# Kernel tuning notes

Hardware: AMD Instinct MI355X
Metric: run time of the kernel (lower is better)

Reference implementation:

```python
import jax, jax.numpy as jnp
import numpy as np

B, N, D = 4, 4096, 1024
DFF = 4 * D
K = 2048  # max(1, int(N * 0.5))


def setup_inputs() -> dict:
    key = jax.random.key(0)
    ks = jax.random.split(key, 4)
    x = jax.random.normal(ks[0], (B, N, D), dtype=jnp.float32)
    gate_w = jax.random.normal(ks[1], (1, D), dtype=jnp.float32) * 0.02
    w1 = jax.random.normal(ks[2], (D, DFF), dtype=jnp.float32) * (1.0 / np.sqrt(D))
    b1 = jnp.zeros((DFF,), dtype=jnp.float32)
    w2 = jax.random.normal(ks[3], (DFF, D), dtype=jnp.float32) * (1.0 / np.sqrt(DFF))
    b2 = jnp.zeros((D,), dtype=jnp.float32)
    return {"x": x, "gate_w": gate_w, "w1": w1, "b1": b1, "w2": w2, "b2": b2, "k": K}


def reference(x, gate_w, w1, b1, w2, b2, k):
    # scores: [B, N] = gate(x).squeeze(-1)
    scores = jnp.einsum("bnd,d->bn", x, gate_w[0])
    _, topk = jax.lax.top_k(scores, k)          # [B, k] token indices
    # gather selected tokens: [B, k, D]
    x_sel = jnp.take_along_axis(x, topk[:, :, None], axis=1)
    # ffn (d -> 4d -> d, GELU) + residual on selected tokens only
    h = jax.nn.gelu(x_sel @ w1 + b1) @ w2 + b2
    x_proc = x_sel + h
    # scatter processed tokens back into a copy of x
    b_idx = jnp.arange(x.shape[0])[:, None]      # [B, 1]
    out = x.at[b_idx, topk].set(x_proc)
    return out
```

## Files before the change

### kernel.cpp

```cpp
#include <hip/hip_runtime.h>
#include <math.h>

#define B_   4
#define N_   4096
#define D_   1024
#define DFF_ 4096
#define K_   2048

typedef __attribute__((ext_vector_type(8))) short short8;
typedef __attribute__((ext_vector_type(4))) float float4v;

__device__ __forceinline__ unsigned short f2bf(float f) {
    unsigned int u = __float_as_uint(f);
    u = (u + 0x7fffu + ((u >> 16) & 1u)) >> 16;
    return (unsigned short)u;
}

__device__ __forceinline__ void gld16(const void* g, void* l) {
    __builtin_amdgcn_global_load_lds((const __attribute__((address_space(1))) void*)g,
                                     (__attribute__((address_space(3))) void*)l, 16, 0, 0);
}

__global__ __launch_bounds__(256) void scores_kernel(const float* __restrict__ x,
                                                     const float* __restrict__ gate_w,
                                                     float* __restrict__ scores,
                                                     int* __restrict__ slot) {
    int wave = (blockIdx.x * blockDim.x + threadIdx.x) >> 6;
    int lane = threadIdx.x & 63;
    if (wave >= B_ * N_) return;
    if (lane == 1) slot[wave] = -1;
    const float4* xr = (const float4*)(x + (size_t)wave * D_);
    const float4* g  = (const float4*)gate_w;
    float acc = 0.f;
    #pragma unroll
    for (int j = 0; j < D_ / 4 / 64; ++j) {
        float4 a = xr[lane + j * 64];
        float4 b = g[lane + j * 64];
        acc += a.x * b.x + a.y * b.y + a.z * b.z + a.w * b.w;
    }
    #pragma unroll
    for (int off = 32; off > 0; off >>= 1) acc += __shfl_down(acc, off, 64);
    if (lane == 0) scores[wave] = acc;
}

__global__ __launch_bounds__(1024) void select_topk_kernel(const float* __restrict__ scores,
                                                           int* __restrict__ topk,
                                                           int* __restrict__ slot) {
    __shared__ unsigned key[N_];
    __shared__ unsigned hist[256];
    __shared__ int sh_bin, sh_rem, sh_ngt;
    __shared__ int wsum[16], woff[16];
    int b = blockIdx.x, tid = threadIdx.x;
    int lane = tid & 63, wid = tid >> 6;

    for (int i = tid; i < N_; i += 1024) {
        unsigned u = __float_as_uint(scores[b * N_ + i]);
        key[i] = (u & 0x80000000u) ? ~u : (u | 0x80000000u);
    }
    if (tid == 0) sh_ngt = 0;
    __syncthreads();

    unsigned prefix = 0, pmask = 0;
    int rem = K_;
    for (int shift = 24; shift >= 0; shift -= 8) {
        if (tid < 256) hist[tid] = 0;
        __syncthreads();
        for (int i = tid; i < N_; i += 1024) {
            unsigned k = key[i];
            if ((k & pmask) == prefix) atomicAdd(&hist[(k >> shift) & 255u], 1u);
        }
        __syncthreads();
        if (tid < 64) {
            unsigned v0 = hist[4 * lane], v1 = hist[4 * lane + 1];
            unsigned v2 = hist[4 * lane + 2], v3 = hist[4 * lane + 3];
            unsigned s3 = v3, s2 = v2 + s3, s1 = v1 + s2, s0 = v0 + s1;
            unsigned t = s0;
            #pragma unroll
            for (int off = 1; off < 64; off <<= 1) {
                unsigned u = __shfl_down(t, off, 64);
                if (lane + off < 64) t += u;
            }
            unsigned above = t - s0;
            unsigned S0 = s0 + above, S1 = s1 + above, S2 = s2 + above, S3 = s3 + above;
            unsigned R = (unsigned)rem;
            if (S0 >= R && S1 < R) { sh_bin = 4 * lane;     sh_rem = rem - (int)S1; }
            if (S1 >= R && S2 < R) { sh_bin = 4 * lane + 1; sh_rem = rem - (int)S2; }
            if (S2 >= R && S3 < R) { sh_bin = 4 * lane + 2; sh_rem = rem - (int)S3; }
            if (S3 >= R && above < R) { sh_bin = 4 * lane + 3; sh_rem = rem - (int)above; }
        }
        __syncthreads();
        prefix |= ((unsigned)sh_bin) << shift;
        pmask  |= 0xffu << shift;
        rem = sh_rem;
    }
    unsigned T = prefix;
    int c_gt = K_ - rem;

    for (int i = tid; i < N_; i += 1024) {
        bool p = key[i] > T;
        unsigned long long m = __ballot(p);
        int cnt = __popcll(m);
        int basepos = 0;
        if (lane == 0 && cnt) basepos = atomicAdd(&sh_ngt, cnt);
        basepos = __shfl(basepos, 0, 64);
        if (p) {
            int pos = basepos + __popcll(m & ((1ULL << lane) - 1ULL));
            topk[b * K_ + pos] = i;
            slot[b * N_ + i] = b * K_ + pos;
        }
    }
    int base = tid * 4, c = 0;
    #pragma unroll
    for (int j = 0; j < 4; ++j) c += (key[base + j] == T);
    int sc = c;
    #pragma unroll
    for (int off = 1; off < 64; off <<= 1) {
        int u = __shfl_up(sc, off, 64);
        if (lane >= off) sc += u;
    }
    if (lane == 63) wsum[wid] = sc;
    __syncthreads();
    if (tid == 0) {
        int run = 0;
        #pragma unroll
        for (int j = 0; j < 16; ++j) { woff[j] = run; run += wsum[j]; }
    }
    __syncthreads();
    int r = woff[wid] + sc - c;
    #pragma unroll
    for (int j = 0; j < 4; ++j) {
        if (key[base + j] == T) {
            if (r < rem) {
                topk[b * K_ + c_gt + r] = base + j;
                slot[b * N_ + base + j] = b * K_ + c_gt + r;
            }
            ++r;
        }
    }
}

__global__ __launch_bounds__(256) void gather_copy_kernel(const float* __restrict__ x,
                                                          const int* __restrict__ slot,
                                                          unsigned short* __restrict__ xsel,
                                                          float* __restrict__ out) {
    int row = blockIdx.x;
    int t = threadIdx.x;
    int s = slot[row];
    float4 v = ((const float4*)(x + (size_t)row * D_))[t];
    if (s >= 0) {
        ushort4 o;
        o.x = f2bf(v.x); o.y = f2bf(v.y); o.z = f2bf(v.z); o.w = f2bf(v.w);
        ((ushort4*)(xsel + (size_t)s * D_))[t] = o;
    } else {
        ((float4*)(out + (size_t)row * D_))[t] = v;
    }
}

__global__ __launch_bounds__(256) void transpose_both_kernel(const float* __restrict__ w1,
                                                             const float* __restrict__ w2,
                                                             unsigned short* __restrict__ w1t,
                                                             unsigned short* __restrict__ w2t) {
    __shared__ float tile[32][33];
    int bid = blockIdx.x;
    const float* src; unsigned short* dst; int R, C, bx, by;
    if (bid < 4096) { src = w1; dst = w1t; R = D_;   C = DFF_; bx = bid & 127;          by = bid >> 7; }
    else            { src = w2; dst = w2t; R = DFF_; C = D_;   bx = (bid - 4096) & 31;  by = (bid - 4096) >> 5; }
    int tx = threadIdx.x & 31, ty = threadIdx.x >> 5;
    int c = bx * 32 + tx, r0 = by * 32;
    #pragma unroll
    for (int j = ty; j < 32; j += 8) tile[j][tx] = src[(size_t)(r0 + j) * C + c];
    __syncthreads();
    int dc = by * 32 + tx, dr0 = bx * 32;
    #pragma unroll
    for (int j = ty; j < 32; j += 8) dst[(size_t)(dr0 + j) * R + dc] = f2bf(tile[tx][j]);
}

__global__ __launch_bounds__(512, 2) void ffn1_pipe_kernel(const unsigned short* __restrict__ A,
                                                           const unsigned short* __restrict__ Bt,
                                                           const float* __restrict__ b1,
                                                           unsigned short* __restrict__ h1) {
    constexpr int K  = D_;
    constexpr int NT = K / 32;
    __shared__ __align__(16) unsigned short smem[65536];

    const int t    = threadIdx.x;
    const int lane = t & 63;
    const int wid  = t >> 6;
    const int quad = lane >> 4;
    const int lr   = lane & 15;
    const int wr   = wid >> 2;
    const int wc   = wid & 3;
    const int row0 = blockIdx.x * 256;
    const int col0 = blockIdx.y * 256;

    const int ch0 = t, ch1 = t + 512;
    const int r0 = ch0 >> 2, c0 = (ch0 & 3) ^ (r0 & 3);
    const int r1 = ch1 >> 2, c1 = (ch1 & 3) ^ (r1 & 3);
    const char* aS0 = (const char*)A  + ((size_t)(row0 + r0) * K + (size_t)c0 * 8) * 2;
    const char* aS1 = (const char*)A  + ((size_t)(row0 + r1) * K + (size_t)c1 * 8) * 2;
    const char* bS0 = (const char*)Bt + ((size_t)(col0 + r0) * K + (size_t)c0 * 8) * 2;
    const char* bS1 = (const char*)Bt + ((size_t)(col0 + r1) * K + (size_t)c1 * 8) * 2;
    const int oA0 = ch0 * 8, oA1 = ch1 * 8;
    const int oB0 = 8192 + ch0 * 8, oB1 = 8192 + ch1 * 8;

    const int sw   = ((quad ^ (lr & 3)) * 8);
    const int aoff = (wr * 128 + lr) * 32 + sw;
    const int boff = 8192 + (wc * 64 + lr) * 32 + sw;

    #pragma unroll
    for (int pt = 0; pt < 3; ++pt) {
        unsigned short* buf = smem + pt * 16384;
        gld16(aS0, buf + oA0); gld16(aS1, buf + oA1);
        gld16(bS0, buf + oB0); gld16(bS1, buf + oB1);
        aS0 += 64; aS1 += 64; bS0 += 64; bS1 += 64;
    }
    asm volatile("s_waitcnt vmcnt(8)" ::: "memory");
    __builtin_amdgcn_s_barrier();

    float4v acc[8][4] = {};
    short8 af[8], bq[4];

    #pragma unroll 4
    for (int kt = 0; kt < NT; ++kt) {
        unsigned short* cur = smem + (kt & 3) * 16384;
        unsigned short* nxt = smem + ((kt + 3) & 3) * 16384;
        const bool pf = (kt + 3 < NT);

        #pragma unroll
        for (int mi = 0; mi < 4; ++mi) af[mi] = *(const short8*)(cur + aoff + mi * 512);
        #pragma unroll
        for (int ni = 0; ni < 4; ++ni) bq[ni] = *(const short8*)(cur + boff + ni * 512);
        if (pf) { gld16(aS0, nxt + oA0); gld16(aS1, nxt + oA1); }
        __builtin_amdgcn_s_barrier();
        __builtin_amdgcn_s_setprio(1);
        #pragma unroll
        for (int mi = 0; mi < 4; ++mi)
            #pragma unroll
            for (int ni = 0; ni < 4; ++ni)
                acc[mi][ni] = __builtin_amdgcn_mfma_f32_16x16x32_bf16(af[mi], bq[ni], acc[mi][ni], 0, 0, 0);
        __builtin_amdgcn_s_setprio(0);
        __builtin_amdgcn_s_barrier();

        #pragma unroll
        for (int mi = 4; mi < 8; ++mi) af[mi] = *(const short8*)(cur + aoff + mi * 512);
        if (pf) { gld16(bS0, nxt + oB0); gld16(bS1, nxt + oB1); }
        aS0 += 64; aS1 += 64; bS0 += 64; bS1 += 64;
        if (kt < NT - 3)       asm volatile("s_waitcnt vmcnt(8)" ::: "memory");
        else if (kt == NT - 3) asm volatile("s_waitcnt vmcnt(4)" ::: "memory");
        else                   asm volatile("s_waitcnt vmcnt(0)" ::: "memory");
        __builtin_amdgcn_s_barrier();
        __builtin_amdgcn_s_setprio(1);
        #pragma unroll
        for (int mi = 4; mi < 8; ++mi)
            #pragma unroll
            for (int ni = 0; ni < 4; ++ni)
                acc[mi][ni] = __builtin_amdgcn_mfma_f32_16x16x32_bf16(af[mi], bq[ni], acc[mi][ni], 0, 0, 0);
        __builtin_amdgcn_s_setprio(0);
        __builtin_amdgcn_s_barrier();
    }

    float bias[4];
    #pragma unroll
    for (int ni = 0; ni < 4; ++ni) bias[ni] = b1[col0 + wc * 64 + ni * 16 + lr];
    unsigned short* ws_ = smem + wid * 5120;
    const int ro = row0 + wr * 128;
    const int co = col0 + wc * 64;
    #pragma unroll
    for (int p = 0; p < 2; ++p) {
        #pragma unroll
        for (int mi = 0; mi < 8; ++mi)
            #pragma unroll
            for (int nj = 0; nj < 2; ++nj) {
                const int ni = p * 2 + nj;
                #pragma unroll
                for (int r = 0; r < 4; ++r) {
                    float u = acc[mi][ni][r] + bias[ni];
                    float tt = 1.5957691216057308f * u * (1.0f + 0.044715f * u * u);
                    float g = u / (1.0f + __expf(-tt));
                    ws_[(mi * 16 + quad * 4 + r) * 40 + nj * 16 + lr] = f2bf(g);
                }
            }
        asm volatile("s_waitcnt lgkmcnt(0)" ::: "memory");
        #pragma unroll
        for (int j = 0; j < 8; ++j) {
            const int chk = lane + j * 64;
            const int rr = chk >> 2, cc = chk & 3;
            short8 v = *(const short8*)(ws_ + rr * 40 + cc * 8);
            *(short8*)(h1 + (size_t)(ro + rr) * DFF_ + co + p * 32 + cc * 8) = v;
        }
        asm volatile("s_waitcnt lgkmcnt(0)" ::: "memory");
    }
}

__global__ __launch_bounds__(256) void ffn2_mfma_kernel(const unsigned short* __restrict__ A,
                                                        const unsigned short* __restrict__ Bt,
                                                        const float* __restrict__ b2,
                                                        const float* __restrict__ x,
                                                        const int* __restrict__ topk,
                                                        float* __restrict__ out) {
    constexpr int K = DFF_;
    __shared__ __align__(16) unsigned short As[128 * 32];
    __shared__ __align__(16) unsigned short Bs[128 * 32];
    int t = threadIdx.x;
    int w = t >> 6, lane = t & 63;
    int quad = lane >> 4, lr = lane & 15;
    int wm = w >> 1, wn = w & 1;
    int row0 = blockIdx.x * 128, col0 = blockIdx.y * 128;

    const char* ga0 = (const char*)(A + (size_t)(row0 + (t >> 2)) * K) + (t & 3) * 16;
    const char* ga1 = ga0 + (size_t)64 * K * 2;
    const char* gb0 = (const char*)(Bt + (size_t)(col0 + (t >> 2)) * K) + (t & 3) * 16;
    const char* gb1 = gb0 + (size_t)64 * K * 2;
    unsigned short* la0 = As + t * 8;   unsigned short* la1 = As + 2048 + t * 8;
    unsigned short* lb0 = Bs + t * 8;   unsigned short* lb1 = Bs + 2048 + t * 8;

    float4v acc[4][4] = {};
    for (int k0 = 0; k0 < K; k0 += 32) {
        gld16(ga0, la0); gld16(ga1, la1);
        gld16(gb0, lb0); gld16(gb1, lb1);
        ga0 += 64; ga1 += 64; gb0 += 64; gb1 += 64;
        __syncthreads();
        short8 af[4], bfv[4];
        #pragma unroll
        for (int mi = 0; mi < 4; ++mi)
            af[mi] = *(const short8*)(As + (size_t)(wm * 64 + mi * 16 + lr) * 32 + quad * 8);
        #pragma unroll
        for (int ni = 0; ni < 4; ++ni)
            bfv[ni] = *(const short8*)(Bs + (size_t)(wn * 64 + ni * 16 + lr) * 32 + quad * 8);
        #pragma unroll
        for (int mi = 0; mi < 4; ++mi)
            #pragma unroll
            for (int ni = 0; ni < 4; ++ni)
                acc[mi][ni] = __builtin_amdgcn_mfma_f32_16x16x32_bf16(af[mi], bfv[ni], acc[mi][ni], 0, 0, 0);
        __syncthreads();
    }

    #pragma unroll
    for (int mi = 0; mi < 4; ++mi) {
        #pragma unroll
        for (int r = 0; r < 4; ++r) {
            int row = row0 + wm * 64 + mi * 16 + quad * 4 + r;
            int gb = row >> 11;
            int tok = topk[row];
            size_t base = ((size_t)(gb * N_ + tok)) * D_;
            #pragma unroll
            for (int ni = 0; ni < 4; ++ni) {
                int col = col0 + wn * 64 + ni * 16 + lr;
                out[base + col] = x[base + col] + acc[mi][ni][r] + b2[col];
            }
        }
    }
}

extern "C" void kernel_launch(void* const* d_in, const int* in_sizes, int n_in,
                              void* d_out, int out_size, void* d_ws, size_t ws_size,
                              hipStream_t stream) {
    const float* x      = (const float*)d_in[0];
    const float* gate_w = (const float*)d_in[1];
    const float* w1     = (const float*)d_in[2];
    const float* b1     = (const float*)d_in[3];
    const float* w2     = (const float*)d_in[4];
    const float* b2     = (const float*)d_in[5];
    float* out = (float*)d_out;

    char* ws = (char*)d_ws;
    float*          scores = (float*)ws;
    int*            topk   = (int*)(ws + (64 << 10));
    int*            slot   = (int*)(ws + (96 << 10));
    unsigned short* xsel   = (unsigned short*)(ws + (160 << 10));
    unsigned short* w1t    = (unsigned short*)(ws + (160 << 10) + (16 << 20));
    unsigned short* w2t    = (unsigned short*)(ws + (160 << 10) + (24 << 20));
    unsigned short* h1     = (unsigned short*)(ws + (160 << 10) + (32 << 20));

    scores_kernel<<<(B_ * N_) / 4, 256, 0, stream>>>(x, gate_w, scores, slot);
    select_topk_kernel<<<B_, 1024, 0, stream>>>(scores, topk, slot);

    transpose_both_kernel<<<8192, 256, 0, stream>>>(w1, w2, w1t, w2t);

    gather_copy_kernel<<<B_ * N_, 256, 0, stream>>>(x, slot, xsel, out);

    ffn1_pipe_kernel<<<dim3(32, 16), 512, 0, stream>>>(xsel, w1t, b1, h1);
    ffn2_mfma_kernel<<<dim3(64, 8), 256, 0, stream>>>(h1, w2t, b2, x, topk, out);
}
```

Baseline: 348.3 us.

## Pipeline FFN2 GEMM with 4-stage LDS ring and new LDS swizzle

```diff
diff --git a/kernel.cpp b/kernel.cpp
--- a/kernel.cpp
+++ b/kernel.cpp
@@ -175,6 +175,7 @@
     for (int j = ty; j < 32; j += 8) dst[(size_t)(dr0 + j) * R + dc] = f2bf(tile[tx][j]);
 }
 
+
 __global__ __launch_bounds__(512, 2) void ffn1_pipe_kernel(const unsigned short* __restrict__ A,
                                                            const unsigned short* __restrict__ Bt,
                                                            const float* __restrict__ b1,
@@ -194,18 +195,21 @@
     const int col0 = blockIdx.y * 256;
 
     const int ch0 = t, ch1 = t + 512;
-    const int r0 = ch0 >> 2, c0 = (ch0 & 3) ^ (r0 & 3);
-    const int r1 = ch1 >> 2, c1 = (ch1 & 3) ^ (r1 & 3);
-    const char* aS0 = (const char*)A  + ((size_t)(row0 + r0) * K + (size_t)c0 * 8) * 2;
-    const char* aS1 = (const char*)A  + ((size_t)(row0 + r1) * K + (size_t)c1 * 8) * 2;
-    const char* bS0 = (const char*)Bt + ((size_t)(col0 + r0) * K + (size_t)c0 * 8) * 2;
-    const char* bS1 = (const char*)Bt + ((size_t)(col0 + r1) * K + (size_t)c1 * 8) * 2;
+    const int rp0 = ch0 >> 3, w0 = (ch0 & 7) ^ (rp0 & 7);
+    const int rp1 = ch1 >> 3, w1 = (ch1 & 7) ^ (rp1 & 7);
+    const int gr0 = rp0 * 2 + (w0 >> 2), gc0 = w0 & 3;
+    const int gr1 = rp1 * 2 + (w1 >> 2), gc1 = w1 & 3;
+    const char* aS0 = (const char*)A  + ((size_t)(row0 + gr0) * K + (size_t)gc0 * 8) * 2;
+    const char* aS1 = (const char*)A  + ((size_t)(row0 + gr1) * K + (size_t)gc1 * 8) * 2;
+    const char* bS0 = (const char*)Bt + ((size_t)(col0 + gr0) * K + (size_t)gc0 * 8) * 2;
+    const char* bS1 = (const char*)Bt + ((size_t)(col0 + gr1) * K + (size_t)gc1 * 8) * 2;
     const int oA0 = ch0 * 8, oA1 = ch1 * 8;
     const int oB0 = 8192 + ch0 * 8, oB1 = 8192 + ch1 * 8;
 
-    const int sw   = ((quad ^ (lr & 3)) * 8);
-    const int aoff = (wr * 128 + lr) * 32 + sw;
-    const int boff = 8192 + (wc * 64 + lr) * 32 + sw;
+    const int rbA = wr * 128 + lr, rA2 = rbA >> 1;
+    const int aoff = (rA2 * 8 + ((((rbA & 1) << 2) | quad) ^ (rA2 & 7))) * 8;
+    const int rbB = wc * 64 + lr, rB2 = rbB >> 1;
+    const int boff = 8192 + (rB2 * 8 + ((((rbB & 1) << 2) | quad) ^ (rB2 & 7))) * 8;
 
     #pragma unroll
     for (int pt = 0; pt < 3; ++pt) {
@@ -292,60 +296,104 @@
     }
 }
 
-__global__ __launch_bounds__(256) void ffn2_mfma_kernel(const unsigned short* __restrict__ A,
-                                                        const unsigned short* __restrict__ Bt,
-                                                        const float* __restrict__ b2,
-                                                        const float* __restrict__ x,
-                                                        const int* __restrict__ topk,
-                                                        float* __restrict__ out) {
-    constexpr int K = DFF_;
-    __shared__ __align__(16) unsigned short As[128 * 32];
-    __shared__ __align__(16) unsigned short Bs[128 * 32];
-    int t = threadIdx.x;
-    int w = t >> 6, lane = t & 63;
-    int quad = lane >> 4, lr = lane & 15;
-    int wm = w >> 1, wn = w & 1;
-    int row0 = blockIdx.x * 128, col0 = blockIdx.y * 128;
-
-    const char* ga0 = (const char*)(A + (size_t)(row0 + (t >> 2)) * K) + (t & 3) * 16;
-    const char* ga1 = ga0 + (size_t)64 * K * 2;
-    const char* gb0 = (const char*)(Bt + (size_t)(col0 + (t >> 2)) * K) + (t & 3) * 16;
-    const char* gb1 = gb0 + (size_t)64 * K * 2;
-    unsigned short* la0 = As + t * 8;   unsigned short* la1 = As + 2048 + t * 8;
-    unsigned short* lb0 = Bs + t * 8;   unsigned short* lb1 = Bs + 2048 + t * 8;
+__global__ __launch_bounds__(512, 2) void ffn2_pipe_kernel(const unsigned short* __restrict__ A,
+                                                           const unsigned short* __restrict__ Bt,
+                                                           const float* __restrict__ b2,
+                                                           const float* __restrict__ x,
+                                                           const int* __restrict__ topk,
+                                                           float* __restrict__ out) {
+    constexpr int K  = DFF_;
+    constexpr int NT = K / 32;
+    __shared__ __align__(16) unsigned short smem[49152];
+
+    const int t    = threadIdx.x;
+    const int lane = t & 63;
+    const int wid  = t >> 6;
+    const int quad = lane >> 4;
+    const int lr   = lane & 15;
+    const int wr   = wid >> 2;
+    const int wc   = wid & 3;
+    const int row0 = blockIdx.x * 128;
+    const int col0 = blockIdx.y * 256;
+
+    const int chA = t;
+    const int rpa = chA >> 3, wa = (chA & 7) ^ (rpa & 7);
+    const char* aS = (const char*)A + ((size_t)(row0 + rpa * 2 + (wa >> 2)) * K + (size_t)(wa & 3) * 8) * 2;
+    const int ch0 = t, ch1 = t + 512;
+    const int rp0 = ch0 >> 3, w0 = (ch0 & 7) ^ (rp0 & 7);
+    const int rp1 = ch1 >> 3, w1 = (ch1 & 7) ^ (rp1 & 7);
+    const char* bS0 = (const char*)Bt + ((size_t)(col0 + rp0 * 2 + (w0 >> 2)) * K + (size_t)(w0 & 3) * 8) * 2;
+    const char* bS1 = (const char*)Bt + ((size_t)(col0 + rp1 * 2 + (w1 >> 2)) * K + (size_t)(w1 & 3) * 8) * 2;
+    const int oA = chA * 8;
+    const int oB0 = 4096 + ch0 * 8, oB1 = 4096 + ch1 * 8;
+
+    const int rbA = wr * 64 + lr, rA2 = rbA >> 1;
+    const int aoff = (rA2 * 8 + ((((rbA & 1) << 2) | quad) ^ (rA2 & 7))) * 8;
+    const int rbB = wc * 64 + lr, rB2 = rbB >> 1;
+    const int boff = 4096 + (rB2 * 8 + ((((rbB & 1) << 2) | quad) ^ (rB2 & 7))) * 8;
+
+    #pragma unroll
+    for (int pt = 0; pt < 3; ++pt) {
+        unsigned short* buf = smem + pt * 12288;
+        gld16(aS, buf + oA); gld16(bS0, buf + oB0); gld16(bS1, buf + oB1);
+        aS += 64; bS0 += 64; bS1 += 64;
+    }
+    asm volatile("s_waitcnt vmcnt(6)" ::: "memory");
+    __builtin_amdgcn_s_barrier();
 
     float4v acc[4][4] = {};
-    for (int k0 = 0; k0 < K; k0 += 32) {
-        gld16(ga0, la0); gld16(ga1, la1);
-        gld16(gb0, lb0); gld16(gb1, lb1);
-        ga0 += 64; ga1 += 64; gb0 += 64; gb1 += 64;
-        __syncthreads();
-        short8 af[4], bfv[4];
-        #pragma unroll
-        for (int mi = 0; mi < 4; ++mi)
-            af[mi] = *(const short8*)(As + (size_t)(wm * 64 + mi * 16 + lr) * 32 + quad * 8);
-        #pragma unroll
-        for (int ni = 0; ni < 4; ++ni)
-            bfv[ni] = *(const short8*)(Bs + (size_t)(wn * 64 + ni * 16 + lr) * 32 + quad * 8);
-        #pragma unroll
-        for (int mi = 0; mi < 4; ++mi)
+    short8 af[4], bq[4];
+
+    #pragma unroll 4
+    for (int kt = 0; kt < NT; ++kt) {
+        unsigned short* cur = smem + (kt & 3) * 12288;
+        unsigned short* nxt = smem + ((kt + 3) & 3) * 12288;
+        const bool pf = (kt + 3 < NT);
+
+        af[0] = *(const short8*)(cur + aoff);
+        af[1] = *(const short8*)(cur + aoff + 512);
+        #pragma unroll
+        for (int ni = 0; ni < 4; ++ni) bq[ni] = *(const short8*)(cur + boff + ni * 512);
+        if (pf) { gld16(aS, nxt + oA); gld16(bS0, nxt + oB0); }
+        __builtin_amdgcn_s_barrier();
+        __builtin_amdgcn_s_setprio(1);
+        #pragma unroll
+        for (int mi = 0; mi < 2; ++mi)
             #pragma unroll
             for (int ni = 0; ni < 4; ++ni)
-                acc[mi][ni] = __builtin_amdgcn_mfma_f32_16x16x32_bf16(af[mi], bfv[ni], acc[mi][ni], 0, 0, 0);
-        __syncthreads();
+                acc[mi][ni] = __builtin_amdgcn_mfma_f32_16x16x32_bf16(af[mi], bq[ni], acc[mi][ni], 0, 0, 0);
+        __builtin_amdgcn_s_setprio(0);
+        __builtin_amdgcn_s_barrier();
+
+        af[2] = *(const short8*)(cur + aoff + 1024);
+        af[3] = *(const short8*)(cur + aoff + 1536);
+        if (pf) { gld16(bS1, nxt + oB1); }
+        aS += 64; bS0 += 64; bS1 += 64;
+        if (kt < NT - 3)       asm volatile("s_waitcnt vmcnt(6)" ::: "memory");
+        else if (kt == NT - 3) asm volatile("s_waitcnt vmcnt(3)" ::: "memory");
+        else                   asm volatile("s_waitcnt vmcnt(0)" ::: "memory");
+        __builtin_amdgcn_s_barrier();
+        __builtin_amdgcn_s_setprio(1);
+        #pragma unroll
+        for (int mi = 2; mi < 4; ++mi)
+            #pragma unroll
+            for (int ni = 0; ni < 4; ++ni)
+                acc[mi][ni] = __builtin_amdgcn_mfma_f32_16x16x32_bf16(af[mi], bq[ni], acc[mi][ni], 0, 0, 0);
+        __builtin_amdgcn_s_setprio(0);
+        __builtin_amdgcn_s_barrier();
     }
 
     #pragma unroll
     for (int mi = 0; mi < 4; ++mi) {
         #pragma unroll
         for (int r = 0; r < 4; ++r) {
-            int row = row0 + wm * 64 + mi * 16 + quad * 4 + r;
+            int row = row0 + wr * 64 + mi * 16 + quad * 4 + r;
             int gb = row >> 11;
             int tok = topk[row];
             size_t base = ((size_t)(gb * N_ + tok)) * D_;
             #pragma unroll
             for (int ni = 0; ni < 4; ++ni) {
-                int col = col0 + wn * 64 + ni * 16 + lr;
+                int col = col0 + wc * 64 + ni * 16 + lr;
                 out[base + col] = x[base + col] + acc[mi][ni][r] + b2[col];
             }
         }
@@ -380,5 +428,5 @@
     gather_copy_kernel<<<B_ * N_, 256, 0, stream>>>(x, slot, xsel, out);
 
     ffn1_pipe_kernel<<<dim3(32, 16), 512, 0, stream>>>(xsel, w1t, b1, h1);
-    ffn2_mfma_kernel<<<dim3(64, 8), 256, 0, stream>>>(h1, w2t, b2, x, topk, out);
-}
+    ffn2_pipe_kernel<<<dim3(64, 4), 512, 0, stream>>>(h1, w2t, b2, x, topk, out);
+}
```

Result: faster. 335.4 us (-3.7%).
